# Optimization experiments

Hardware: AMD Instinct MI355X
Metric: run time of the kernel (lower is better)

Reference implementation:

```python
import jax, jax.numpy as jnp
import numpy as np

H = 16
D = 1024
HD = D // H

def setup_inputs() -> dict:
    key = jax.random.key(0)
    ks = jax.random.split(key, 5)
    x = jax.random.normal(ks[0], (2, 2048, D), dtype=jnp.float32)
    w_qkv = jax.random.normal(ks[1], (D, 3 * D), dtype=jnp.float32) / np.sqrt(D)
    b_qkv = jax.random.normal(ks[2], (3 * D,), dtype=jnp.float32) * 0.01
    w_o = jax.random.normal(ks[3], (D, D), dtype=jnp.float32) / np.sqrt(D)
    b_o = jax.random.normal(ks[4], (D,), dtype=jnp.float32) * 0.01
    return {"x": x, "w_qkv": w_qkv, "b_qkv": b_qkv, "w_o": w_o, "b_o": b_o}

def reference(x, w_qkv, b_qkv, w_o, b_o):
    b, s, d = x.shape
    qkv = x @ w_qkv + b_qkv                      # [b, s, 3d]
    q, k, v = jnp.split(qkv, 3, axis=-1)
    q = q.reshape(b, s, H, HD)
    k = k.reshape(b, s, H, HD)
    v = v.reshape(b, s, H, HD)
    scores = jnp.einsum('bqhd,bkhd->bhqk', q, k) / jnp.sqrt(jnp.float32(HD))
    attn = jax.nn.softmax(scores, axis=-1)       # [b, h, s, s]
    out = jnp.einsum('bhqk,bkhd->bqhd', attn, v).reshape(b, s, d)
    return out @ w_o + b_o
```

## Files before the change

kernel.cpp:

```cpp
#include <hip/hip_runtime.h>
#include <hip/hip_bf16.h>

typedef unsigned int u32;
typedef unsigned short u16;
typedef __attribute__((ext_vector_type(8))) short bf16x8;
typedef __attribute__((ext_vector_type(4))) float f32x4;
typedef __attribute__((ext_vector_type(16))) float f32x16;
typedef __attribute__((ext_vector_type(8))) u16 u16x8;
typedef __attribute__((ext_vector_type(2))) u32 u32x2;
typedef __attribute__((ext_vector_type(4))) u32 u32x4;

#define MFMA16(A, B, C) __builtin_amdgcn_mfma_f32_16x16x32_bf16(A, B, C, 0, 0, 0)
#define MFMA32(A, B, C) __builtin_amdgcn_mfma_f32_32x32x16_bf16(A, B, C, 0, 0, 0)

#define C_SCALE 0.1803368801111244f

__device__ __forceinline__ u16 f2bf(float f) {
  __hip_bfloat16 h = __float2bfloat16(f);
  u16 u;
  __builtin_memcpy(&u, &h, 2);
  return u;
}

__device__ __forceinline__ u32 pk2(float a, float b) {
  return (u32)f2bf(a) | ((u32)f2bf(b) << 16);
}

__device__ __forceinline__ float exp2fast(float x) {
#if __has_builtin(__builtin_amdgcn_exp2f)
  return __builtin_amdgcn_exp2f(x);
#else
  return exp2f(x);
#endif
}

__device__ __forceinline__ u32x2 pl32swap(u32 a, u32 b) {
  return __builtin_amdgcn_permlane32_swap(a, b, false, false);
}

__device__ __forceinline__ void g2l16(const void* g, void* l) {
  __builtin_amdgcn_global_load_lds(
      (const __attribute__((address_space(1))) u32*)g,
      (__attribute__((address_space(3))) u32*)l, 16, 0, 0);
}

__global__ __launch_bounds__(256) void xcvt(const float* __restrict__ in,
                                            u16* __restrict__ out, int n8) {
  const int i = blockIdx.x * 256 + threadIdx.x;
  if (i >= n8) return;
  const float4* p = (const float4*)in + (size_t)i * 2;
  const float4 a = p[0], b = p[1];
  u16x8 o;
  o[0] = f2bf(a.x); o[1] = f2bf(a.y); o[2] = f2bf(a.z); o[3] = f2bf(a.w);
  o[4] = f2bf(b.x); o[5] = f2bf(b.y); o[6] = f2bf(b.z); o[7] = f2bf(b.w);
  *((u16x8*)out + i) = o;
}

__global__ __launch_bounds__(256) void wtrans(const float* __restrict__ in,
                                              u16* __restrict__ out, int R, int C,
                                              int scale_n, float scale) {
  __shared__ float t[32][33];
  const int r0 = blockIdx.y << 5, c0 = blockIdx.x << 5;
  const int tr = threadIdx.x >> 3, tc = (threadIdx.x & 7) << 2;
  const float4 v = *(const float4*)(in + (size_t)(r0 + tr) * C + c0 + tc);
  t[tr][tc] = v.x; t[tr][tc + 1] = v.y; t[tr][tc + 2] = v.z; t[tr][tc + 3] = v.w;
  __syncthreads();
  const float s = (c0 + tr < scale_n) ? scale : 1.f;
  u32 p0 = pk2(t[tc][tr] * s, t[tc + 1][tr] * s);
  u32 p1 = pk2(t[tc + 2][tr] * s, t[tc + 3][tr] * s);
  u32* dst = (u32*)(out + (size_t)(c0 + tr) * R + r0 + tc);
  dst[0] = p0;
  dst[1] = p1;
}

template <int OUT_BF16>
__global__ __launch_bounds__(256) void gemm_mfma(
    const u16* __restrict__ A, const u16* __restrict__ Bt,
    const float* __restrict__ bias, void* __restrict__ Cv, int N, int K,
    int bsn, float bsc) {
  __shared__ u16 As[128 * 32];
  __shared__ u16 Bs[128 * 32];
  const int tid = threadIdx.x;
  const int l = tid & 63, g = l >> 4, lr = l & 15;
  const int w = tid >> 6;
  const int wm = (w >> 1) << 6, wn = (w & 1) << 6;
  const int bm = blockIdx.y << 7, bn = blockIdx.x << 7;

  f32x4 acc[4][4];
  const f32x4 zero = {0.f, 0.f, 0.f, 0.f};
#pragma unroll
  for (int i = 0; i < 4; ++i)
#pragma unroll
    for (int j = 0; j < 4; ++j) acc[i][j] = zero;

  const int bi0 = tid, bi1 = 256 + tid;
  const int r0 = bi0 >> 2, lb0 = (bi0 & 3) ^ ((r0 >> 1) & 3);
  const int r1 = bi1 >> 2, lb1 = (bi1 & 3) ^ ((r1 >> 1) & 3);
  const u16* a0 = A + (size_t)(bm + r0) * K + lb0 * 8;
  const u16* a1 = A + (size_t)(bm + r1) * K + lb1 * 8;
  const u16* b0 = Bt + (size_t)(bn + r0) * K + lb0 * 8;
  const u16* b1 = Bt + (size_t)(bn + r1) * K + lb1 * 8;

  const int swA = (lr >> 1) & 3;
  const int aoff = (wm + lr) * 64 + ((g ^ swA) << 4);
  const int boff = (wn + lr) * 64 + ((g ^ swA) << 4);

  for (int k0 = 0; k0 < K; k0 += 32) {
    __syncthreads();
    g2l16(a0 + k0, (char*)As + bi0 * 16);
    g2l16(a1 + k0, (char*)As + bi1 * 16);
    g2l16(b0 + k0, (char*)Bs + bi0 * 16);
    g2l16(b1 + k0, (char*)Bs + bi1 * 16);
    __syncthreads();
    bf16x8 af[4], bfv[4];
#pragma unroll
    for (int mi = 0; mi < 4; ++mi)
      af[mi] = *(const bf16x8*)((const char*)As + aoff + mi * 1024);
#pragma unroll
    for (int ni = 0; ni < 4; ++ni)
      bfv[ni] = *(const bf16x8*)((const char*)Bs + boff + ni * 1024);
#pragma unroll
    for (int mi = 0; mi < 4; ++mi)
#pragma unroll
      for (int ni = 0; ni < 4; ++ni)
        acc[mi][ni] = MFMA16(af[mi], bfv[ni], acc[mi][ni]);
  }

  float bv[4];
#pragma unroll
  for (int ni = 0; ni < 4; ++ni) {
    const int col = bn + wn + ni * 16 + lr;
    bv[ni] = bias[col] * (col < bsn ? bsc : 1.f);
  }
  const int crow = bm + wm + (g << 2);
  const int ccol = bn + wn + lr;
  if (OUT_BF16) {
    u16* C = (u16*)Cv;
#pragma unroll
    for (int mi = 0; mi < 4; ++mi)
#pragma unroll
      for (int ni = 0; ni < 4; ++ni)
#pragma unroll
        for (int j = 0; j < 4; ++j)
          C[(size_t)(crow + mi * 16 + j) * N + ccol + ni * 16] =
              f2bf(acc[mi][ni][j] + bv[ni]);
  } else {
    float* C = (float*)Cv;
#pragma unroll
    for (int mi = 0; mi < 4; ++mi)
#pragma unroll
      for (int ni = 0; ni < 4; ++ni)
#pragma unroll
        for (int j = 0; j < 4; ++j)
          C[(size_t)(crow + mi * 16 + j) * N + ccol + ni * 16] =
              acc[mi][ni][j] + bv[ni];
  }
}

__global__ __launch_bounds__(256) void vtrans(const u16* __restrict__ qkvb,
                                              u16* __restrict__ vt) {
  const int wid = (blockIdx.x << 2) + (threadIdx.x >> 6);
  const int l = threadIdx.x & 63;
  const int dc = wid & 7, st = (wid >> 3) & 31, h = (wid >> 8) & 15, b = wid >> 12;
  const int s = (st << 6) + l;
  const u16x8 v = *(const u16x8*)(qkvb + (size_t)(b * 2048 + s) * 3072 + 2048 + h * 64 + dc * 8);
  u16* dst = vt + ((size_t)(((b << 4) + h) << 6) + (dc << 3)) * 2048 + s;
#pragma unroll
  for (int j = 0; j < 8; ++j) dst[(size_t)j * 2048] = v[j];
}

__global__ __launch_bounds__(256, 2) void attn_mfma(
    const u16* __restrict__ qkvb, const u16* __restrict__ vt,
    u16* __restrict__ attnb) {
  __shared__ u16 Qs[128 * 64];
  __shared__ u16 Ks[64 * 64];
  __shared__ u16 Vs[64 * 64];

  const int qt = blockIdx.x, head = blockIdx.y, b = blockIdx.z;
  const int tid = threadIdx.x, w = tid >> 6, l = tid & 63;
  const int lq = l & 31, hw = l >> 5;
  const size_t sb = (size_t)b * 2048;
  const f32x16 z16 = {};

  {
    const u16* qb = qkvb + (sb + (size_t)qt * 128) * 3072 + head * 64;
#pragma unroll
    for (int j = 0; j < 4; ++j) {
      const int qi = tid + 256 * j;
      const int r = qi >> 3, blk = (qi & 7) ^ (r & 7);
      g2l16(qb + (size_t)r * 3072 + blk * 8, (char*)Qs + qi * 16);
    }
  }
  const int bi0 = tid, bi1 = 256 + tid;
  const int sr0 = bi0 >> 3, slb0 = (bi0 & 7) ^ (sr0 & 7);
  const int sr1 = bi1 >> 3, slb1 = (bi1 & 7) ^ (sr1 & 7);

  __syncthreads();
  bf16x8 qf[4];
  {
    const int row = (w << 5) + lq;
#pragma unroll
    for (int dc = 0; dc < 4; ++dc)
      qf[dc] = *(const bf16x8*)((const char*)Qs + row * 128 +
                                (((2 * dc + hw) ^ (row & 7)) << 4));
  }

  float m_run = -1e30f, l_run = 0.f;
  f32x16 o0 = z16, o1 = z16;

  const u16* kbase = qkvb + sb * 3072 + 1024 + head * 64;
  const u16* vbase = vt + ((size_t)((b << 4) + head) << 6) * 2048;

  for (int kt = 0; kt < 32; ++kt) {
    __syncthreads();
    const size_t ko = (size_t)kt << 6;
    g2l16(kbase + (ko + sr0) * 3072 + slb0 * 8, (char*)Ks + bi0 * 16);
    g2l16(kbase + (ko + sr1) * 3072 + slb1 * 8, (char*)Ks + bi1 * 16);
    g2l16(vbase + (size_t)sr0 * 2048 + ko + slb0 * 8, (char*)Vs + bi0 * 16);
    g2l16(vbase + (size_t)sr1 * 2048 + ko + slb1 * 8, (char*)Vs + bi1 * 16);
    __syncthreads();

    f32x16 st0 = z16, st1 = z16;
#pragma unroll
    for (int dc = 0; dc < 4; ++dc) {
      const int blk = 2 * dc + hw;
      const bf16x8 k0 = *(const bf16x8*)((const char*)Ks + lq * 128 +
                                         ((blk ^ (lq & 7)) << 4));
      st0 = MFMA32(k0, qf[dc], st0);
      const bf16x8 k1 = *(const bf16x8*)((const char*)Ks + (32 + lq) * 128 +
                                         ((blk ^ (lq & 7)) << 4));
      st1 = MFMA32(k1, qf[dc], st1);
    }

    float mx = st0[0];
#pragma unroll
    for (int i = 1; i < 16; ++i) mx = fmaxf(mx, st0[i]);
#pragma unroll
    for (int i = 0; i < 16; ++i) mx = fmaxf(mx, st1[i]);
    {
      const u32x2 r = pl32swap(__float_as_uint(mx), __float_as_uint(mx));
      mx = fmaxf(__uint_as_float(r.x), __uint_as_float(r.y));
    }
    if (!__all(mx - m_run <= 8.f)) {
      const float m_new = fmaxf(m_run, mx);
      const float resc = exp2fast(m_run - m_new);
      float rs[16];
#pragma unroll
      for (int r = 0; r < 16; ++r)
        rs[r] = __shfl(resc, (r & 3) + 8 * (r >> 2) + 4 * hw);
#pragma unroll
      for (int r = 0; r < 16; ++r) { o0[r] *= rs[r]; o1[r] *= rs[r]; }
      l_run *= resc;
      m_run = m_new;
    }
    float lsum = 0.f;
#pragma unroll
    for (int i = 0; i < 16; ++i) { st0[i] = exp2fast(st0[i] - m_run); lsum += st0[i]; }
#pragma unroll
    for (int i = 0; i < 16; ++i) { st1[i] = exp2fast(st1[i] - m_run); lsum += st1[i]; }
    {
      const u32x2 r = pl32swap(__float_as_uint(lsum), __float_as_uint(lsum));
      lsum = __uint_as_float(r.x) + __uint_as_float(r.y);
    }
    l_run += lsum;

    bf16x8 pa[4];
#pragma unroll
    for (int kc = 0; kc < 4; ++kc) {
      const f32x16 s = (kc < 2) ? st0 : st1;
      const int q0 = (kc & 1) * 8;
      const u32 W01 = pk2(s[q0 + 0], s[q0 + 1]);
      const u32 W23 = pk2(s[q0 + 2], s[q0 + 3]);
      const u32 W45 = pk2(s[q0 + 4], s[q0 + 5]);
      const u32 W67 = pk2(s[q0 + 6], s[q0 + 7]);
      const u32x2 rA = pl32swap(W01, W45);
      const u32x2 rB = pl32swap(W23, W67);
      const u32x4 wds = {rA.x, rB.x, rA.y, rB.y};
      pa[kc] = __builtin_bit_cast(bf16x8, wds);
    }

#pragma unroll
    for (int kc = 0; kc < 4; ++kc) {
      const int blk = 2 * kc + hw;
      const bf16x8 v0 = *(const bf16x8*)((const char*)Vs + lq * 128 +
                                         ((blk ^ (lq & 7)) << 4));
      o0 = MFMA32(pa[kc], v0, o0);
      const bf16x8 v1 = *(const bf16x8*)((const char*)Vs + (32 + lq) * 128 +
                                         ((blk ^ (lq & 7)) << 4));
      o1 = MFMA32(pa[kc], v1, o1);
    }
  }

  const float invl = 1.f / l_run;
  u16* ob = attnb + (sb + (size_t)qt * 128 + (w << 5)) * 1024 + head * 64;
#pragma unroll
  for (int r = 0; r < 16; ++r) {
    const int qo = (r & 3) + 8 * (r >> 2) + 4 * hw;
    const float iv = __shfl(invl, qo);
    ob[(size_t)qo * 1024 + lq] = f2bf(o0[r] * iv);
    ob[(size_t)qo * 1024 + 32 + lq] = f2bf(o1[r] * iv);
  }
}

extern "C" void kernel_launch(void* const* d_in, const int* in_sizes, int n_in,
                              void* d_out, int out_size, void* d_ws, size_t ws_size,
                              hipStream_t stream) {
  const float* x     = (const float*)d_in[0];
  const float* w_qkv = (const float*)d_in[1];
  const float* b_qkv = (const float*)d_in[2];
  const float* w_o   = (const float*)d_in[3];
  const float* b_o   = (const float*)d_in[4];
  float* out = (float*)d_out;

  u16* xb    = (u16*)d_ws;
  u16* wqkvt = xb + (size_t)4096 * 1024;
  u16* wot   = wqkvt + (size_t)3072 * 1024;
  u16* qkvb  = wot + (size_t)1024 * 1024;
  u16* vtb   = qkvb + (size_t)4096 * 3072;
  u16* attnb = vtb + (size_t)2 * 16 * 64 * 2048;

  xcvt<<<dim3(2048), dim3(256), 0, stream>>>(x, xb, 4096 * 1024 / 8);
  wtrans<<<dim3(96, 32), dim3(256), 0, stream>>>(w_qkv, wqkvt, 1024, 3072, 1024, C_SCALE);
  wtrans<<<dim3(32, 32), dim3(256), 0, stream>>>(w_o, wot, 1024, 1024, 0, 1.f);

  gemm_mfma<1><<<dim3(24, 32), dim3(256), 0, stream>>>(xb, wqkvt, b_qkv, qkvb, 3072, 1024, 1024, C_SCALE);

  vtrans<<<dim3(2048), dim3(256), 0, stream>>>(qkvb, vtb);
  attn_mfma<<<dim3(16, 16, 2), dim3(256), 0, stream>>>(qkvb, vtb, attnb);

  gemm_mfma<0><<<dim3(8, 32), dim3(256), 0, stream>>>(attnb, wot, b_o, out, 1024, 1024, 0, 1.f);
}
```

Measured before the change: 142.5 us.

## Double-buffer K/V tiles in attention loop and defer row-sum reduction

The attention kernel now keeps two LDS buffers for K and V and issues the loads for the next key tile before computing on the current one. This replaces the two barriers per iteration with one at the end, so global-to-LDS latency can overlap with the MFMA and softmax work. The per-iteration cross-lane reduction of the row sum is moved to after the loop, which is valid because the rescaling is linear. MFMA sections are also wrapped in s_setprio. LDS use per block grows by 16 KB, which may affect occupancy at two blocks per CU.

New measurement: 145.3 us. Within noise of the previous version (+1.9%).

```diff
diff --git a/kernel.cpp b/kernel.cpp
--- a/kernel.cpp
+++ b/kernel.cpp
@@ -173,8 +173,8 @@
     const u16* __restrict__ qkvb, const u16* __restrict__ vt,
     u16* __restrict__ attnb) {
   __shared__ u16 Qs[128 * 64];
-  __shared__ u16 Ks[64 * 64];
-  __shared__ u16 Vs[64 * 64];
+  __shared__ u16 Ks[2][64 * 64];
+  __shared__ u16 Vs[2][64 * 64];
 
   const int qt = blockIdx.x, head = blockIdx.y, b = blockIdx.z;
   const int tid = threadIdx.x, w = tid >> 6, l = tid & 63;
@@ -182,6 +182,27 @@
   const size_t sb = (size_t)b * 2048;
   const f32x16 z16 = {};
 
+  const int bi0 = tid, bi1 = 256 + tid;
+  const int sr0 = bi0 >> 3, slb0 = (bi0 & 7) ^ (sr0 & 7);
+  const int sr1 = bi1 >> 3, slb1 = (bi1 & 7) ^ (sr1 & 7);
+
+  const u16* kbase = qkvb + sb * 3072 + 1024 + head * 64;
+  const u16* vbase = vt + ((size_t)((b << 4) + head) << 6) * 2048;
+
+  const u16* kp0 = kbase + (size_t)sr0 * 3072 + slb0 * 8;
+  const u16* kp1 = kbase + (size_t)sr1 * 3072 + slb1 * 8;
+  const u16* vp0 = vbase + (size_t)sr0 * 2048 + slb0 * 8;
+  const u16* vp1 = vbase + (size_t)sr1 * 2048 + slb1 * 8;
+
+#define STAGE(buf, kt)                                                        \
+  do {                                                                        \
+    const size_t ko_ = (size_t)(kt) << 6;                                     \
+    g2l16(kp0 + ko_ * 3072, (char*)Ks[buf] + bi0 * 16);                       \
+    g2l16(kp1 + ko_ * 3072, (char*)Ks[buf] + bi1 * 16);                       \
+    g2l16(vp0 + ko_, (char*)Vs[buf] + bi0 * 16);                              \
+    g2l16(vp1 + ko_, (char*)Vs[buf] + bi1 * 16);                              \
+  } while (0)
+
   {
     const u16* qb = qkvb + (sb + (size_t)qt * 128) * 3072 + head * 64;
 #pragma unroll
@@ -191,11 +212,9 @@
       g2l16(qb + (size_t)r * 3072 + blk * 8, (char*)Qs + qi * 16);
     }
   }
-  const int bi0 = tid, bi1 = 256 + tid;
-  const int sr0 = bi0 >> 3, slb0 = (bi0 & 7) ^ (sr0 & 7);
-  const int sr1 = bi1 >> 3, slb1 = (bi1 & 7) ^ (sr1 & 7);
-
+  STAGE(0, 0);
   __syncthreads();
+
   bf16x8 qf[4];
   {
     const int row = (w << 5) + lq;
@@ -208,29 +227,23 @@
   float m_run = -1e30f, l_run = 0.f;
   f32x16 o0 = z16, o1 = z16;
 
-  const u16* kbase = qkvb + sb * 3072 + 1024 + head * 64;
-  const u16* vbase = vt + ((size_t)((b << 4) + head) << 6) * 2048;
-
   for (int kt = 0; kt < 32; ++kt) {
-    __syncthreads();
-    const size_t ko = (size_t)kt << 6;
-    g2l16(kbase + (ko + sr0) * 3072 + slb0 * 8, (char*)Ks + bi0 * 16);
-    g2l16(kbase + (ko + sr1) * 3072 + slb1 * 8, (char*)Ks + bi1 * 16);
-    g2l16(vbase + (size_t)sr0 * 2048 + ko + slb0 * 8, (char*)Vs + bi0 * 16);
-    g2l16(vbase + (size_t)sr1 * 2048 + ko + slb1 * 8, (char*)Vs + bi1 * 16);
-    __syncthreads();
+    const int cur = kt & 1;
+    if (kt < 31) STAGE(cur ^ 1, kt + 1);
 
     f32x16 st0 = z16, st1 = z16;
+    __builtin_amdgcn_s_setprio(1);
 #pragma unroll
     for (int dc = 0; dc < 4; ++dc) {
       const int blk = 2 * dc + hw;
-      const bf16x8 k0 = *(const bf16x8*)((const char*)Ks + lq * 128 +
+      const bf16x8 k0 = *(const bf16x8*)((const char*)Ks[cur] + lq * 128 +
                                          ((blk ^ (lq & 7)) << 4));
       st0 = MFMA32(k0, qf[dc], st0);
-      const bf16x8 k1 = *(const bf16x8*)((const char*)Ks + (32 + lq) * 128 +
+      const bf16x8 k1 = *(const bf16x8*)((const char*)Ks[cur] + (32 + lq) * 128 +
                                          ((blk ^ (lq & 7)) << 4));
       st1 = MFMA32(k1, qf[dc], st1);
     }
+    __builtin_amdgcn_s_setprio(0);
 
     float mx = st0[0];
 #pragma unroll
@@ -258,10 +271,6 @@
     for (int i = 0; i < 16; ++i) { st0[i] = exp2fast(st0[i] - m_run); lsum += st0[i]; }
 #pragma unroll
     for (int i = 0; i < 16; ++i) { st1[i] = exp2fast(st1[i] - m_run); lsum += st1[i]; }
-    {
-      const u32x2 r = pl32swap(__float_as_uint(lsum), __float_as_uint(lsum));
-      lsum = __uint_as_float(r.x) + __uint_as_float(r.y);
-    }
     l_run += lsum;
 
     bf16x8 pa[4];
@@ -279,18 +288,27 @@
       pa[kc] = __builtin_bit_cast(bf16x8, wds);
     }
 
+    __builtin_amdgcn_s_setprio(1);
 #pragma unroll
     for (int kc = 0; kc < 4; ++kc) {
       const int blk = 2 * kc + hw;
-      const bf16x8 v0 = *(const bf16x8*)((const char*)Vs + lq * 128 +
+      const bf16x8 v0 = *(const bf16x8*)((const char*)Vs[cur] + lq * 128 +
                                          ((blk ^ (lq & 7)) << 4));
       o0 = MFMA32(pa[kc], v0, o0);
-      const bf16x8 v1 = *(const bf16x8*)((const char*)Vs + (32 + lq) * 128 +
+      const bf16x8 v1 = *(const bf16x8*)((const char*)Vs[cur] + (32 + lq) * 128 +
                                          ((blk ^ (lq & 7)) << 4));
       o1 = MFMA32(pa[kc], v1, o1);
     }
-  }
-
+    __builtin_amdgcn_s_setprio(0);
+
+    __syncthreads();
+  }
+#undef STAGE
+
+  {
+    const u32x2 r = pl32swap(__float_as_uint(l_run), __float_as_uint(l_run));
+    l_run = __uint_as_float(r.x) + __uint_as_float(r.y);
+  }
   const float invl = 1.f / l_run;
   u16* ob = attnb + (sb + (size_t)qt * 128 + (w << 5)) * 1024 + head * 64;
 #pragma unroll
```

## Load two K/V tiles per barrier pair and defer row-sum lane reduction

Applied to the files above, without the earlier changes.

The attention loop now stages two 64-key K and V tiles into LDS per iteration, so it runs 16 iterations with half as many barrier pairs. The two tiles are processed one after the other inside the loop. Per-tile lane-swap reduction of the softmax row sum is moved to a single reduction after the loop, and K/V address arithmetic is hoisted out of the loop. LDS use grows by 16 KB per block, which may reduce occupancy. Tiles are still not prefetched while compute runs.

Result: no change. 141.8 us (-0.5%).

```diff
diff --git a/kernel.cpp b/kernel.cpp
--- a/kernel.cpp
+++ b/kernel.cpp
@@ -173,8 +173,8 @@
     const u16* __restrict__ qkvb, const u16* __restrict__ vt,
     u16* __restrict__ attnb) {
   __shared__ u16 Qs[128 * 64];
-  __shared__ u16 Ks[64 * 64];
-  __shared__ u16 Vs[64 * 64];
+  __shared__ u16 Ks2[2][64 * 64];
+  __shared__ u16 Vs2[2][64 * 64];
 
   const int qt = blockIdx.x, head = blockIdx.y, b = blockIdx.z;
   const int tid = threadIdx.x, w = tid >> 6, l = tid & 63;
@@ -182,6 +182,18 @@
   const size_t sb = (size_t)b * 2048;
   const f32x16 z16 = {};
 
+  const int bi0 = tid, bi1 = 256 + tid;
+  const int sr0 = bi0 >> 3, slb0 = (bi0 & 7) ^ (sr0 & 7);
+  const int sr1 = bi1 >> 3, slb1 = (bi1 & 7) ^ (sr1 & 7);
+
+  const u16* kbase = qkvb + sb * 3072 + 1024 + head * 64;
+  const u16* vbase = vt + ((size_t)((b << 4) + head) << 6) * 2048;
+
+  const u16* kp0 = kbase + (size_t)sr0 * 3072 + slb0 * 8;
+  const u16* kp1 = kbase + (size_t)sr1 * 3072 + slb1 * 8;
+  const u16* vp0 = vbase + (size_t)sr0 * 2048 + slb0 * 8;
+  const u16* vp1 = vbase + (size_t)sr1 * 2048 + slb1 * 8;
+
   {
     const u16* qb = qkvb + (sb + (size_t)qt * 128) * 3072 + head * 64;
 #pragma unroll
@@ -191,11 +203,8 @@
       g2l16(qb + (size_t)r * 3072 + blk * 8, (char*)Qs + qi * 16);
     }
   }
-  const int bi0 = tid, bi1 = 256 + tid;
-  const int sr0 = bi0 >> 3, slb0 = (bi0 & 7) ^ (sr0 & 7);
-  const int sr1 = bi1 >> 3, slb1 = (bi1 & 7) ^ (sr1 & 7);
-
   __syncthreads();
+
   bf16x8 qf[4];
   {
     const int row = (w << 5) + lq;
@@ -208,89 +217,92 @@
   float m_run = -1e30f, l_run = 0.f;
   f32x16 o0 = z16, o1 = z16;
 
-  const u16* kbase = qkvb + sb * 3072 + 1024 + head * 64;
-  const u16* vbase = vt + ((size_t)((b << 4) + head) << 6) * 2048;
-
-  for (int kt = 0; kt < 32; ++kt) {
+  for (int kt = 0; kt < 16; ++kt) {
+    const size_t ko = (size_t)kt << 7;
     __syncthreads();
-    const size_t ko = (size_t)kt << 6;
-    g2l16(kbase + (ko + sr0) * 3072 + slb0 * 8, (char*)Ks + bi0 * 16);
-    g2l16(kbase + (ko + sr1) * 3072 + slb1 * 8, (char*)Ks + bi1 * 16);
-    g2l16(vbase + (size_t)sr0 * 2048 + ko + slb0 * 8, (char*)Vs + bi0 * 16);
-    g2l16(vbase + (size_t)sr1 * 2048 + ko + slb1 * 8, (char*)Vs + bi1 * 16);
+    g2l16(kp0 + ko * 3072, (char*)Ks2[0] + bi0 * 16);
+    g2l16(kp1 + ko * 3072, (char*)Ks2[0] + bi1 * 16);
+    g2l16(kp0 + (ko + 64) * 3072, (char*)Ks2[1] + bi0 * 16);
+    g2l16(kp1 + (ko + 64) * 3072, (char*)Ks2[1] + bi1 * 16);
+    g2l16(vp0 + ko, (char*)Vs2[0] + bi0 * 16);
+    g2l16(vp1 + ko, (char*)Vs2[0] + bi1 * 16);
+    g2l16(vp0 + ko + 64, (char*)Vs2[1] + bi0 * 16);
+    g2l16(vp1 + ko + 64, (char*)Vs2[1] + bi1 * 16);
     __syncthreads();
 
-    f32x16 st0 = z16, st1 = z16;
-#pragma unroll
-    for (int dc = 0; dc < 4; ++dc) {
-      const int blk = 2 * dc + hw;
-      const bf16x8 k0 = *(const bf16x8*)((const char*)Ks + lq * 128 +
-                                         ((blk ^ (lq & 7)) << 4));
-      st0 = MFMA32(k0, qf[dc], st0);
-      const bf16x8 k1 = *(const bf16x8*)((const char*)Ks + (32 + lq) * 128 +
-                                         ((blk ^ (lq & 7)) << 4));
-      st1 = MFMA32(k1, qf[dc], st1);
+#pragma unroll
+    for (int sub = 0; sub < 2; ++sub) {
+      const char* Kt = (const char*)Ks2[sub];
+      const char* Vt = (const char*)Vs2[sub];
+
+      f32x16 st0 = z16, st1 = z16;
+#pragma unroll
+      for (int dc = 0; dc < 4; ++dc) {
+        const int blk = 2 * dc + hw;
+        const bf16x8 k0 = *(const bf16x8*)(Kt + lq * 128 + ((blk ^ (lq & 7)) << 4));
+        st0 = MFMA32(k0, qf[dc], st0);
+        const bf16x8 k1 = *(const bf16x8*)(Kt + (32 + lq) * 128 + ((blk ^ (lq & 7)) << 4));
+        st1 = MFMA32(k1, qf[dc], st1);
+      }
+
+      float mx = st0[0];
+#pragma unroll
+      for (int i = 1; i < 16; ++i) mx = fmaxf(mx, st0[i]);
+#pragma unroll
+      for (int i = 0; i < 16; ++i) mx = fmaxf(mx, st1[i]);
+      {
+        const u32x2 r = pl32swap(__float_as_uint(mx), __float_as_uint(mx));
+        mx = fmaxf(__uint_as_float(r.x), __uint_as_float(r.y));
+      }
+      if (!__all(mx - m_run <= 8.f)) {
+        const float m_new = fmaxf(m_run, mx);
+        const float resc = exp2fast(m_run - m_new);
+        float rs[16];
+#pragma unroll
+        for (int r = 0; r < 16; ++r)
+          rs[r] = __shfl(resc, (r & 3) + 8 * (r >> 2) + 4 * hw);
+#pragma unroll
+        for (int r = 0; r < 16; ++r) { o0[r] *= rs[r]; o1[r] *= rs[r]; }
+        l_run *= resc;
+        m_run = m_new;
+      }
+      float lsum = 0.f;
+#pragma unroll
+      for (int i = 0; i < 16; ++i) { st0[i] = exp2fast(st0[i] - m_run); lsum += st0[i]; }
+#pragma unroll
+      for (int i = 0; i < 16; ++i) { st1[i] = exp2fast(st1[i] - m_run); lsum += st1[i]; }
+      l_run += lsum;
+
+      bf16x8 pa[4];
+#pragma unroll
+      for (int kc = 0; kc < 4; ++kc) {
+        const f32x16 s = (kc < 2) ? st0 : st1;
+        const int q0 = (kc & 1) * 8;
+        const u32 W01 = pk2(s[q0 + 0], s[q0 + 1]);
+        const u32 W23 = pk2(s[q0 + 2], s[q0 + 3]);
+        const u32 W45 = pk2(s[q0 + 4], s[q0 + 5]);
+        const u32 W67 = pk2(s[q0 + 6], s[q0 + 7]);
+        const u32x2 rA = pl32swap(W01, W45);
+        const u32x2 rB = pl32swap(W23, W67);
+        const u32x4 wds = {rA.x, rB.x, rA.y, rB.y};
+        pa[kc] = __builtin_bit_cast(bf16x8, wds);
+      }
+
+#pragma unroll
+      for (int kc = 0; kc < 4; ++kc) {
+        const int blk = 2 * kc + hw;
+        const bf16x8 v0 = *(const bf16x8*)(Vt + lq * 128 + ((blk ^ (lq & 7)) << 4));
+        o0 = MFMA32(pa[kc], v0, o0);
+        const bf16x8 v1 = *(const bf16x8*)(Vt + (32 + lq) * 128 + ((blk ^ (lq & 7)) << 4));
+        o1 = MFMA32(pa[kc], v1, o1);
+      }
     }
-
-    float mx = st0[0];
-#pragma unroll
-    for (int i = 1; i < 16; ++i) mx = fmaxf(mx, st0[i]);
-#pragma unroll
-    for (int i = 0; i < 16; ++i) mx = fmaxf(mx, st1[i]);
-    {
-      const u32x2 r = pl32swap(__float_as_uint(mx), __float_as_uint(mx));
-      mx = fmaxf(__uint_as_float(r.x), __uint_as_float(r.y));
-    }
-    if (!__all(mx - m_run <= 8.f)) {
-      const float m_new = fmaxf(m_run, mx);
-      const float resc = exp2fast(m_run - m_new);
-      float rs[16];
-#pragma unroll
-      for (int r = 0; r < 16; ++r)
-        rs[r] = __shfl(resc, (r & 3) + 8 * (r >> 2) + 4 * hw);
-#pragma unroll
-      for (int r = 0; r < 16; ++r) { o0[r] *= rs[r]; o1[r] *= rs[r]; }
-      l_run *= resc;
-      m_run = m_new;
-    }
-    float lsum = 0.f;
-#pragma unroll
-    for (int i = 0; i < 16; ++i) { st0[i] = exp2fast(st0[i] - m_run); lsum += st0[i]; }
-#pragma unroll
-    for (int i = 0; i < 16; ++i) { st1[i] = exp2fast(st1[i] - m_run); lsum += st1[i]; }
-    {
-      const u32x2 r = pl32swap(__float_as_uint(lsum), __float_as_uint(lsum));
-      lsum = __uint_as_float(r.x) + __uint_as_float(r.y);
-    }
-    l_run += lsum;
-
-    bf16x8 pa[4];
-#pragma unroll
-    for (int kc = 0; kc < 4; ++kc) {
-      const f32x16 s = (kc < 2) ? st0 : st1;
-      const int q0 = (kc & 1) * 8;
-      const u32 W01 = pk2(s[q0 + 0], s[q0 + 1]);
-      const u32 W23 = pk2(s[q0 + 2], s[q0 + 3]);
-      const u32 W45 = pk2(s[q0 + 4], s[q0 + 5]);
-      const u32 W67 = pk2(s[q0 + 6], s[q0 + 7]);
-      const u32x2 rA = pl32swap(W01, W45);
-      const u32x2 rB = pl32swap(W23, W67);
-      const u32x4 wds = {rA.x, rB.x, rA.y, rB.y};
-      pa[kc] = __builtin_bit_cast(bf16x8, wds);
-    }
-
-#pragma unroll
-    for (int kc = 0; kc < 4; ++kc) {
-      const int blk = 2 * kc + hw;
-      const bf16x8 v0 = *(const bf16x8*)((const char*)Vs + lq * 128 +
-                                         ((blk ^ (lq & 7)) << 4));
-      o0 = MFMA32(pa[kc], v0, o0);
-      const bf16x8 v1 = *(const bf16x8*)((const char*)Vs + (32 + lq) * 128 +
-                                         ((blk ^ (lq & 7)) << 4));
-      o1 = MFMA32(pa[kc], v1, o1);
-    }
-  }
-
+  }
+
+  {
+    const u32x2 r = pl32swap(__float_as_uint(l_run), __float_as_uint(l_run));
+    l_run = __uint_as_float(r.x) + __uint_as_float(r.y);
+  }
   const float invl = 1.f / l_run;
   u16* ob = attnb + (sb + (size_t)qt * 128 + (w << 5)) * 1024 + head * 64;
 #pragma unroll
```
